# Kernel tuning notes

Hardware: AMD Instinct MI355X
Metric: run time of the kernel (lower is better)

Reference implementation:

```python
import math
import jax, jax.numpy as jnp
import numpy as np

# CoordinateDescentRouter defaults (lucidrains/CoLT5-attention)
N_ITERS, EPS, EPS_INIT, EPS_DECAY, FETCH_K_RATIO = 20, 0.03, 4.0, 0.7, 9.0 / 8.0

B, N, D, G, H, DH, NQ, NKV = 2, 4096, 1024, 2, 16, 64, 1024, 1024
DIM_INNER = H * DH  # 1024


def coor_descent(s, k):
    # s: (b, g, n). Differentiable top-k relaxation via coordinate descent.
    logk = math.log(k)
    eps_sched = [max(EPS_INIT * EPS_DECAY ** i, EPS) for i in range(N_ITERS + 1)]
    b = -s
    a = jnp.zeros_like(s[..., :1])
    for ce in eps_sched[:-1]:
        sb = (s + b) / ce
        a = ce * (logk - jax.scipy.special.logsumexp(sb, axis=-1, keepdims=True))
        b = -jax.nn.relu(s + a)
    return jnp.exp((s + a + b) / eps_sched[-1])


def route(x, routing_tokens, num_tokens):
    # x: (b,n,d), routing_tokens: (g,d) -> indices (b,g,nt), scores (b,g,nt), routed (b,g,nt,d)
    bsz, n, _ = x.shape
    k_cd = min(int(num_tokens * FETCH_K_RATIO), n)
    sim = jnp.einsum('bnd,gd->bgn', x, routing_tokens)
    scores = coor_descent(sim, k_cd)
    scores, idx = jax.lax.top_k(scores, num_tokens)
    # straight-through: forward value 1.0, gradient flows through coor_descent scores
    scores = scores + jax.lax.stop_gradient(1.0 - scores)
    routed = x[jnp.arange(bsz)[:, None, None], idx]
    return idx, scores, routed


def rmsnorm(t, gamma):
    # t: (b,g,n,d); F.normalize over feature dim * sqrt(d) * gamma (g,d)
    norm = jnp.sqrt(jnp.sum(t * t, axis=-1, keepdims=True))
    return t / jnp.maximum(norm, 1e-12) * math.sqrt(t.shape[-1]) * gamma[None, :, None, :]


def grouped_attention(queries, kvs, v_scale, o_scale, gamma_q, gamma_c, wq, wkv, wo, null_kv):
    bsz, g, nq, d = queries.shape
    h, dh = null_kv.shape[2], null_kv.shape[-1]
    qn = rmsnorm(queries, gamma_q)
    cn = rmsnorm(kvs, gamma_c)
    # grouped 1x1 conv == per-group linear; within-group output channel order is (h, dh)
    q = jnp.einsum('bgnd,ged->bgne', qn, wq)
    kv = jnp.einsum('bgnd,ged->bgne', cn, wkv)
    k, v = jnp.split(kv, 2, axis=-1)

    def to_heads(t):
        return t.reshape(bsz, g, t.shape[2], h, dh).transpose(0, 1, 3, 2, 4)  # (b,g,h,n,dh)

    q, k, v = map(to_heads, (q, k, v))
    v = v * v_scale  # (b,g,1,nkv,1) broadcast, applied before null kv concat
    nk = jnp.broadcast_to(null_kv[0][None], (bsz,) + null_kv[0].shape)
    nv = jnp.broadcast_to(null_kv[1][None], (bsz,) + null_kv[1].shape)
    k = jnp.concatenate([nk, k], axis=-2)
    v = jnp.concatenate([nv, v], axis=-2)
    sim = jnp.einsum('bghnd,bghmd->bghnm', q * dh ** -0.5, k)
    attn = jax.nn.softmax(sim, axis=-1)
    o = jnp.einsum('bghnm,bghmd->bghnd', attn, v)
    o = o.transpose(0, 1, 3, 2, 4).reshape(bsz, g, nq, h * dh)
    o = jnp.einsum('bgne,gde->bgnd', o, wo)
    return o * o_scale


def setup_inputs() -> dict:
    key = jax.random.key(0)
    ks = jax.random.split(key, 8)
    inv = 1.0 / math.sqrt(D)
    return {
        'x': jax.random.normal(ks[0], (B, N, D), jnp.float32),
        'rt_q': jax.random.normal(ks[1], (G, D), jnp.float32),
        'rt_kv': jax.random.normal(ks[2], (G, D), jnp.float32),
        'gamma_q': jnp.ones((G, D), jnp.float32),
        'gamma_c': jnp.ones((G, D), jnp.float32),
        'wq': jax.random.normal(ks[3], (G, DIM_INNER, D), jnp.float32) * inv,
        'wkv': jax.random.normal(ks[4], (G, 2 * DIM_INNER, D), jnp.float32) * inv,
        'wo': jax.random.normal(ks[5], (G, D, DIM_INNER), jnp.float32) * inv,
        'null_kv': jax.random.normal(ks[6], (2, G, H, 1, DH), jnp.float32),
        'null_token': jax.random.normal(ks[7], (1, 1, D), jnp.float32),
        'num_routed_queries': NQ,
        'num_routed_key_values': NKV,
    }


def reference(x, rt_q, rt_kv, gamma_q, gamma_c, wq, wkv, wo, null_kv, null_token,
              num_routed_queries, num_routed_key_values):
    bsz, n, d = x.shape
    q_idx, q_scores, queries = route(x, rt_q, num_routed_queries)
    _, kv_scores, key_values = route(x, rt_kv, num_routed_key_values)
    v_scale = kv_scores[:, :, None, :, None]  # (b,g,1,nkv,1)
    o_scale = q_scores[..., None]             # (b,g,nq,1)
    attn_out = grouped_attention(queries, key_values, v_scale, o_scale,
                                 gamma_q, gamma_c, wq, wkv, wo, null_kv)
    # scatter routed outputs back, averaging over experts that picked each token
    flat_idx = q_idx.reshape(bsz, -1)                 # (b, g*nq)
    flat_out = attn_out.reshape(bsz, -1, d)           # (b, g*nq, d)
    bidx = jnp.arange(bsz)[:, None]
    summed = jnp.zeros_like(x).at[bidx, flat_idx].add(flat_out)
    counts = jnp.zeros((bsz, n), x.dtype).at[bidx, flat_idx].add(1.0)
    not_routed = (counts == 0.0)[..., None]
    summed = jnp.where(not_routed, 0.0, summed)
    out = summed / jnp.maximum(counts[..., None], 1e-5)
    out = jnp.where(not_routed, null_token, out)
    return out
```

## Files before the change

### kernel.cpp

```cpp
#include <hip/hip_runtime.h>

typedef __attribute__((ext_vector_type(8))) short short8;
typedef __attribute__((ext_vector_type(4))) short short4v;
typedef __attribute__((ext_vector_type(4))) float f32x4;

#define B_ 2
#define N_ 4096
#define D_ 1024
#define G_ 2
#define H_ 16
#define DH_ 64
#define NSLOT 1088
#define LOGK 7.0492548412558374f
#define ATTN_SCALE 0.18033688011112043f
#define FIXED_M 32.0f

#define BAR() __builtin_amdgcn_s_barrier()
#define WAITV4 asm volatile("s_waitcnt vmcnt(4)" ::: "memory")
#define WAITV0 asm volatile("s_waitcnt vmcnt(0)" ::: "memory")
#define GLDS(src, dst) __builtin_amdgcn_global_load_lds( \
    (const __attribute__((address_space(1))) void*)(src), \
    (__attribute__((address_space(3))) void*)(dst), 16, 0, 0)

__device__ __forceinline__ float bf2f(short s) {
  return __uint_as_float(((unsigned)(unsigned short)s) << 16);
}
__device__ __forceinline__ short f2bf(float f) {
  unsigned u = __float_as_uint(f);
  u = (u + 0x7FFFu + ((u >> 16) & 1u)) >> 16;
  return (short)u;
}
__device__ __forceinline__ short f2bf_trunc(float f) {
  return (short)(__float_as_uint(f) >> 16);
}

__global__ __launch_bounds__(256) void prep_kernel(
    const float* __restrict__ x, const float* __restrict__ rtq,
    const float* __restrict__ rtkv, float* __restrict__ sim,
    const float* __restrict__ null_kv, short* __restrict__ kb_,
    short* __restrict__ vb_)
{
  int bid = blockIdx.x;
  if (bid < 2048) {
    int wid = threadIdx.x >> 6, lane = threadIdx.x & 63;
    int row = bid * 4 + wid;
    int b = row >> 12, n = row & (N_ - 1);
    const float* xr = x + (size_t)row * D_;
    float a0 = 0.f, a1 = 0.f, a2 = 0.f, a3 = 0.f;
#pragma unroll
    for (int c = 0; c < 4; ++c) {
      int d = c * 256 + lane * 4;
      f32x4 xv = *(const f32x4*)(xr + d);
      f32x4 r0 = *(const f32x4*)(rtq + d);
      f32x4 r1 = *(const f32x4*)(rtq + D_ + d);
      f32x4 r2 = *(const f32x4*)(rtkv + d);
      f32x4 r3 = *(const f32x4*)(rtkv + D_ + d);
#pragma unroll
      for (int e = 0; e < 4; ++e) {
        a0 += xv[e] * r0[e];
        a1 += xv[e] * r1[e];
        a2 += xv[e] * r2[e];
        a3 += xv[e] * r3[e];
      }
    }
#pragma unroll
    for (int o = 32; o; o >>= 1) {
      a0 += __shfl_xor(a0, o); a1 += __shfl_xor(a1, o);
      a2 += __shfl_xor(a2, o); a3 += __shfl_xor(a3, o);
    }
    if (lane == 0) {
      sim[((size_t)(b)*G_ + 0) * N_ + n] = a0;
      sim[((size_t)(b)*G_ + 1) * N_ + n] = a1;
      sim[((size_t)(B_ + b)*G_ + 0) * N_ + n] = a2;
      sim[((size_t)(B_ + b)*G_ + 1) * N_ + n] = a3;
    }
  } else {
    int bgh = (bid - 2048) * 4 + (threadIdx.x >> 6);
    int g = (bgh >> 4) & 1, h = bgh & 15;
    int t = threadIdx.x & 63;
    float kvk = null_kv[((size_t)(0 * G_ + g) * H_ + h) * DH_ + t];
    float kvv = null_kv[((size_t)(1 * G_ + g) * H_ + h) * DH_ + t];
    kb_[((size_t)bgh * NSLOT + 1024) * DH_ + t] = f2bf(kvk);
    vb_[((size_t)bgh * DH_ + t) * NSLOT + 1024] = f2bf(kvv);
  }
}

__global__ __launch_bounds__(1024) void topk_wconv(
    const float* __restrict__ sim, int* __restrict__ idxout, int* __restrict__ inv,
    const float* __restrict__ wq, const float* __restrict__ wkv,
    const float* __restrict__ wo, short* __restrict__ dq,
    short* __restrict__ dkv, short* __restrict__ dwo)
{
  if (blockIdx.x >= 8) {
    int base = (blockIdx.x - 8) * 4096 + threadIdx.x;
#pragma unroll
    for (int c = 0; c < 4; ++c) {
      int i = base + c * 1024;
      const float* src; short* dst;
      if (i < 524288) { src = wq; dst = dq; }
      else if (i < 1572864) { src = wkv; dst = dkv; i -= 524288; }
      else { src = wo; dst = dwo; i -= 1572864; }
      f32x4 v = ((const f32x4*)src)[i];
      short4v o;
#pragma unroll
      for (int e = 0; e < 4; ++e) o[e] = f2bf(v[e]);
      ((short4v*)dst)[i] = o;
    }
    return;
  }

  __shared__ float rbm[16];
  __shared__ float rbs[16];
  __shared__ float res;
  __shared__ unsigned keys[N_];
  __shared__ int scanbuf[16];

  int r = blockIdx.x >> 2, b = (blockIdx.x >> 1) & 1, g = blockIdx.x & 1;
  const float* srow = sim + ((size_t)blockIdx.x << 12);
  int tid = threadIdx.x, lane = tid & 63, wid = tid >> 6;

  float sv[4];
#pragma unroll
  for (int j = 0; j < 4; ++j) sv[j] = srow[tid * 4 + j];

  float a = 0.f;
  double epsd = 4.0;
  for (int it = 0; it < 20; ++it) {
    float eps = (float)fmax(epsd, 0.03);
    epsd *= 0.7;
    float sb[4]; float mt = -INFINITY;
#pragma unroll
    for (int j = 0; j < 4; ++j) {
      float bb = (it == 0) ? (-sv[j]) : (-fmaxf(sv[j] + a, 0.f));
      sb[j] = (sv[j] + bb) / eps;
      mt = fmaxf(mt, sb[j]);
    }
#pragma unroll
    for (int o = 32; o; o >>= 1) mt = fmaxf(mt, __shfl_xor(mt, o));
    float st = 0.f;
#pragma unroll
    for (int j = 0; j < 4; ++j) st += expf(sb[j] - mt);
#pragma unroll
    for (int o = 32; o; o >>= 1) st += __shfl_xor(st, o);
    if (lane == 0) { rbm[wid] = mt; rbs[wid] = st; }
    __syncthreads();
    if (tid < 64) {
      float m2 = (tid < 16) ? rbm[tid] : -INFINITY;
      float s2 = (tid < 16) ? rbs[tid] : 0.f;
#pragma unroll
      for (int o = 8; o; o >>= 1) {
        float mo = __shfl_xor(m2, o), so = __shfl_xor(s2, o);
        float mn = fmaxf(m2, mo);
        s2 = s2 * expf(m2 - mn) + so * expf(mo - mn);
        m2 = mn;
      }
      if (tid == 0) res = logf(s2) + m2;
    }
    __syncthreads();
    float lse = res;
    a = eps * (LOGK - lse);
  }
  __syncthreads();

  unsigned kb[4]; int c1 = 0;
#pragma unroll
  for (int j = 0; j < 4; ++j) {
    float sc = expf(fminf(sv[j] + a, 0.f) / 0.03f);
    kb[j] = __float_as_uint(sc);
    keys[tid * 4 + j] = kb[j];
    c1 += (kb[j] == 0x3F800000u);
  }
#pragma unroll
  for (int o = 32; o; o >>= 1) c1 += __shfl_xor(c1, o);
  if (lane == 0) scanbuf[wid] = c1;
  __syncthreads();
  int c1tot = 0;
  for (int i = 0; i < 16; ++i) c1tot += scanbuf[i];
  __syncthreads();

  int flag[4];
  if (c1tot >= 1024) {
#pragma unroll
    for (int j = 0; j < 4; ++j) flag[j] = (kb[j] == 0x3F800000u);
  } else {
#pragma unroll
    for (int j = 0; j < 4; ++j) {
      unsigned kn = kb[j]; int n = tid * 4 + j; int rank = 0;
      for (int m = 0; m < N_; ++m) {
        unsigned km = keys[m];
        rank += (km > kn) || (km == kn && m < n);
      }
      flag[j] = (rank < 1024);
    }
  }

  int cnt = flag[0] + flag[1] + flag[2] + flag[3];
  int inc = cnt;
#pragma unroll
  for (int o = 1; o < 64; o <<= 1) {
    int tt = __shfl_up(inc, o);
    if (lane >= o) inc += tt;
  }
  if (lane == 63) scanbuf[wid] = inc;
  __syncthreads();
  int off = 0;
  for (int w = 0; w < wid; ++w) off += scanbuf[w];
  int pos = off + inc - cnt;
  int* op = idxout + ((size_t)blockIdx.x << 10);
  int* ip = inv + ((size_t)(b * G_ + g) << 12);
#pragma unroll
  for (int j = 0; j < 4; ++j) {
    if (flag[j]) {
      if (pos < 1024) {
        int n = tid * 4 + j;
        op[pos] = n;
        if (r == 0) ip[n] = pos;
      }
      pos++;
    }
  }
}

__global__ __launch_bounds__(256) void gather_rms(
    const float* __restrict__ x, const int* __restrict__ idx,
    const float* __restrict__ gamma_q, const float* __restrict__ gamma_c,
    short* __restrict__ qn, short* __restrict__ cn)
{
  __shared__ float rb[4];
  __shared__ float tot;
  int id = blockIdx.x;
  int r = id >> 12, rem = id & 4095;
  int g = (rem >> 10) & 1;
  int b = rem >> 11;
  int tok = idx[id];
  int t = threadIdx.x;
  const float* xr = x + ((size_t)b * N_ + tok) * D_;
  f32x4 v = *(const f32x4*)(xr + t * 4);
  float ss = v[0]*v[0] + v[1]*v[1] + v[2]*v[2] + v[3]*v[3];
#pragma unroll
  for (int o = 32; o; o >>= 1) ss += __shfl_xor(ss, o);
  if ((t & 63) == 0) rb[t >> 6] = ss;
  __syncthreads();
  if (t == 0) tot = rb[0] + rb[1] + rb[2] + rb[3];
  __syncthreads();
  float scale = 32.0f / fmaxf(sqrtf(tot), 1e-12f);
  const float* gm = (r ? gamma_c : gamma_q) + g * D_;
  f32x4 gv = *(const f32x4*)(gm + t * 4);
  short* dst = (r ? cn : qn) + ((size_t)rem << 10) + t * 4;
  short4v ov;
#pragma unroll
  for (int e = 0; e < 4; ++e) ov[e] = f2bf(v[e] * scale * gv[e]);
  *(short4v*)dst = ov;
}

__global__ __launch_bounds__(256, 3) void gemm_qkv(
    const short* __restrict__ qn, const short* __restrict__ cn,
    const short* __restrict__ wqb, const short* __restrict__ wkvb,
    short* __restrict__ qout, short* __restrict__ kout, short* __restrict__ vout)
{
  __shared__ short As[8192];
  __shared__ short Bs[8192];
  int t = threadIdx.x, lane = t & 63, wid = t >> 6;
  int grp = lane >> 4, l15 = lane & 15;
  int wm = wid >> 1, wn = wid & 1;
  int lin = blockIdx.x + 8 * (blockIdx.y + 24 * blockIdx.z);
  int s = (lin & 7) * 96 + (lin >> 3);
  int bx = s & 7, ny = (s >> 3) % 24, bg = s / 192;
  bool isq = ny < 8;
  const short* A  = isq ? qn : cn;
  const short* Bw = isq ? wqb : wkvb;
  int NB = isq ? 1024 : 2048;
  int nbase = (isq ? ny : ny - 8) * 128;
  float oscale = isq ? ATTN_SCALE : 1.0f;
  int mbase = bx * 128;
  int g = bg & 1;
  const short* Ab = A + ((size_t)bg << 20);
  const short* Bp = Bw + ((size_t)g * NB + nbase) * 1024;

  f32x4 zero = {0.f, 0.f, 0.f, 0.f};
  f32x4 acc[4][4];
#pragma unroll
  for (int i = 0; i < 4; ++i)
#pragma unroll
    for (int j = 0; j < 4; ++j) acc[i][j] = zero;

  const short* apA[4]; const short* apB[4]; int dstoff[4];
#pragma unroll
  for (int c = 0; c < 4; ++c) {
    int u = c * 256 + t;
    int row = u >> 3, j = u & 7;
    int cu = (j ^ (row & 7)) << 3;
    apA[c] = Ab + ((size_t)(mbase + row) << 10) + cu;
    apB[c] = Bp + ((size_t)row << 10) + cu;
    dstoff[c] = c * 2048 + wid * 512;
  }

  for (int kb = 0; kb < 16; ++kb) {
    int ko = kb * 64;
    if (kb) __syncthreads();
#pragma unroll
    for (int c = 0; c < 4; ++c) {
      GLDS(apA[c] + ko, As + dstoff[c]);
      GLDS(apB[c] + ko, Bs + dstoff[c]);
    }
    WAITV0;
    __syncthreads();
    const char* Ac = (const char*)As;
    const char* Bc = (const char*)Bs;
#pragma unroll
    for (int kf = 0; kf < 2; ++kf) {
      short8 af[4], bf_[4];
#pragma unroll
      for (int mt = 0; mt < 4; ++mt) {
        int ra = wm * 64 + mt * 16 + l15;
        af[mt] = *(const short8*)(Ac + ra * 128 + (((grp << 4) + (kf << 6)) ^ ((ra & 7) << 4)));
      }
#pragma unroll
      for (int nt = 0; nt < 4; ++nt) {
        int rb = wn * 64 + nt * 16 + l15;
        bf_[nt] = *(const short8*)(Bc + rb * 128 + (((grp << 4) + (kf << 6)) ^ ((rb & 7) << 4)));
      }
      __builtin_amdgcn_s_setprio(1);
#pragma unroll
      for (int mt = 0; mt < 4; ++mt)
#pragma unroll
        for (int nt = 0; nt < 4; ++nt)
          acc[mt][nt] = __builtin_amdgcn_mfma_f32_16x16x32_bf16(af[mt], bf_[nt], acc[mt][nt], 0, 0, 0);
      __builtin_amdgcn_s_setprio(0);
    }
  }

#pragma unroll
  for (int mt = 0; mt < 4; ++mt)
#pragma unroll
    for (int nt = 0; nt < 4; ++nt) {
      int n = nbase + wn*64 + nt*16 + l15;
#pragma unroll
      for (int rr = 0; rr < 4; ++rr) {
        int m = mbase + wm*64 + mt*16 + grp*4 + rr;
        float v = acc[mt][nt][rr] * oscale;
        if (isq) {
          qout[((size_t)bg * 1024 + m) * 1024 + n] = f2bf(v);
        } else {
          if (n < 1024) {
            kout[(((size_t)bg * H_ + (n >> 6)) * NSLOT + m) * DH_ + (n & 63)] = f2bf(v);
          } else {
            int e = n - 1024;
            vout[(((size_t)bg * H_ + (e >> 6)) * DH_ + (e & 63)) * NSLOT + m] = f2bf(v);
          }
        }
      }
    }
}

__global__ __launch_bounds__(256, 3) void gemm_wo(
    const short* __restrict__ A, const short* __restrict__ Bw,
    short* __restrict__ out0, short* __restrict__ out1)
{
  __shared__ short As[8192];
  __shared__ short Bs[8192];
  int t = threadIdx.x, lane = t & 63, wid = t >> 6;
  int grp = lane >> 4, l15 = lane & 15;
  int wm = wid >> 1, wn = wid & 1;
  int lin = blockIdx.x + 8 * (blockIdx.y + 8 * blockIdx.z);
  int s = (lin & 7) * 64 + (lin >> 3);
  int mbase = (s & 7) * 128, nbase = ((s >> 3) & 7) * 128;
  int z = s >> 6, bg = z >> 1, sp = z & 1, g = bg & 1;
  short* out = sp ? out1 : out0;
  const short* Ab = A + ((size_t)bg << 20);
  const short* Bp = Bw + ((size_t)g * 1024 + nbase) * 1024;

  f32x4 zero = {0.f, 0.f, 0.f, 0.f};
  f32x4 acc[4][4];
#pragma unroll
  for (int i = 0; i < 4; ++i)
#pragma unroll
    for (int j = 0; j < 4; ++j) acc[i][j] = zero;

  const short* apA[4]; const short* apB[4]; int dstoff[4];
#pragma unroll
  for (int c = 0; c < 4; ++c) {
    int u = c * 256 + t;
    int row = u >> 3, j = u & 7;
    int cu = (j ^ (row & 7)) << 3;
    apA[c] = Ab + ((size_t)(mbase + row) << 10) + cu;
    apB[c] = Bp + ((size_t)row << 10) + cu;
    dstoff[c] = c * 2048 + wid * 512;
  }

  int kb0 = sp * 8;
  for (int kk = 0; kk < 8; ++kk) {
    int ko = (kb0 + kk) * 64;
    if (kk) __syncthreads();
#pragma unroll
    for (int c = 0; c < 4; ++c) {
      GLDS(apA[c] + ko, As + dstoff[c]);
      GLDS(apB[c] + ko, Bs + dstoff[c]);
    }
    WAITV0;
    __syncthreads();
    const char* Ac = (const char*)As;
    const char* Bc = (const char*)Bs;
#pragma unroll
    for (int kf = 0; kf < 2; ++kf) {
      short8 af[4], bf_[4];
#pragma unroll
      for (int mt = 0; mt < 4; ++mt) {
        int ra = wm * 64 + mt * 16 + l15;
        af[mt] = *(const short8*)(Ac + ra * 128 + (((grp << 4) + (kf << 6)) ^ ((ra & 7) << 4)));
      }
#pragma unroll
      for (int nt = 0; nt < 4; ++nt) {
        int rb = wn * 64 + nt * 16 + l15;
        bf_[nt] = *(const short8*)(Bc + rb * 128 + (((grp << 4) + (kf << 6)) ^ ((rb & 7) << 4)));
      }
      __builtin_amdgcn_s_setprio(1);
#pragma unroll
      for (int mt = 0; mt < 4; ++mt)
#pragma unroll
        for (int nt = 0; nt < 4; ++nt)
          acc[mt][nt] = __builtin_amdgcn_mfma_f32_16x16x32_bf16(af[mt], bf_[nt], acc[mt][nt], 0, 0, 0);
      __builtin_amdgcn_s_setprio(0);
    }
  }

#pragma unroll
  for (int mt = 0; mt < 4; ++mt)
#pragma unroll
    for (int nt = 0; nt < 4; ++nt) {
      int n = nbase + wn*64 + nt*16 + l15;
#pragma unroll
      for (int rr = 0; rr < 4; ++rr) {
        int m = mbase + wm*64 + mt*16 + grp*4 + rr;
        out[((size_t)bg * 1024 + m) * 1024 + n] = f2bf(acc[mt][nt][rr]);
      }
    }
}

__global__ __launch_bounds__(256, 3) void attn_kernel(
    const short* __restrict__ q, const short* __restrict__ k,
    const short* __restrict__ vT, short* __restrict__ o0,
    short* __restrict__ o1, float* __restrict__ ml)
{
  __shared__ short Ks[2][4096];
  __shared__ short Vs[2][4096];
  __shared__ short Ps[4][32 * 72];
  int bgh = blockIdx.x, qb = blockIdx.y, sp = blockIdx.z;
  int bg = bgh >> 4, h = bgh & 15;
  int wid = threadIdx.x >> 6, lane = threadIdx.x & 63;
  int l15 = lane & 15, grp = lane >> 4;
  int qbase = qb * 128 + wid * 32;
  short* Pw = &Ps[wid][0];

  short8 bq[2][2];
#pragma unroll
  for (int qh = 0; qh < 2; ++qh) {
    const short* qp = q + ((size_t)bg * 1024 + qbase + qh * 16 + l15) * 1024 + h * 64 + (grp << 3);
    bq[qh][0] = *(const short8*)qp;
    bq[qh][1] = *(const short8*)(qp + 32);
  }
  short8 ones8;
  short ov = (l15 == 0) ? (short)0x3F80 : (short)0;
#pragma unroll
  for (int e = 0; e < 8; ++e) ones8[e] = ov;

  int u0 = wid * 128 + lane, u1 = u0 + 64;
  int r0 = u0 >> 3, j0 = u0 & 7, r1 = u1 >> 3, j1 = u1 & 7;
  const short* kbase = k + (size_t)bgh * NSLOT * DH_;
  const short* vbase = vT + (size_t)bgh * DH_ * NSLOT;
  const short* kss0 = kbase + r0 * 64 + ((j0 ^ (r0 & 7)) << 3);
  const short* kss1 = kbase + r1 * 64 + ((j1 ^ (r1 & 7)) << 3);
  const short* vss0 = vbase + (size_t)r0 * NSLOT + ((j0 ^ (r0 & 7)) << 3);
  const short* vss1 = vbase + (size_t)r1 * NSLOT + ((j1 ^ (r1 & 7)) << 3);

  f32x4 zero = {0.f, 0.f, 0.f, 0.f};
  f32x4 minit = {-FIXED_M, -FIXED_M, -FIXED_M, -FIXED_M};
  f32x4 oacc[2][4], lacc[2];
#pragma unroll
  for (int qh = 0; qh < 2; ++qh) {
    lacc[qh] = zero;
#pragma unroll
    for (int dt = 0; dt < 4; ++dt) oacc[qh][dt] = zero;
  }

  auto STAGE = [&](int tile, int p) {
    size_t ko = (size_t)tile * 4096;
    size_t vo = (size_t)tile * 64;
    short* kd = &Ks[p][0] + wid * 1024;
    short* vd = &Vs[p][0] + wid * 1024;
    GLDS(kss0 + ko, kd);
    GLDS(kss1 + ko, kd + 512);
    GLDS(vss0 + vo, vd);
    GLDS(vss1 + vo, vd + 512);
  };

  auto PROCESS = [&](int tile, int p) {
    const char* Kc = (const char*)&Ks[p][0];
    const char* Vc = (const char*)&Vs[p][0];
    f32x4 sacc[2][4];
#pragma unroll
    for (int qh = 0; qh < 2; ++qh)
#pragma unroll
      for (int kt = 0; kt < 4; ++kt) sacc[qh][kt] = minit;
#pragma unroll
    for (int kf = 0; kf < 2; ++kf) {
      short8 ka[4];
#pragma unroll
      for (int kt = 0; kt < 4; ++kt) {
        int ra = kt * 16 + l15;
        ka[kt] = *(const short8*)(Kc + ra * 128 + (((grp + 4 * kf) ^ (ra & 7)) << 4));
      }
      __builtin_amdgcn_s_setprio(1);
#pragma unroll
      for (int kt = 0; kt < 4; ++kt)
#pragma unroll
        for (int qh = 0; qh < 2; ++qh)
          sacc[qh][kt] = __builtin_amdgcn_mfma_f32_16x16x32_bf16(ka[kt], bq[qh][kf], sacc[qh][kt], 0, 0, 0);
      __builtin_amdgcn_s_setprio(0);
    }
    if (tile == 16) {
#pragma unroll
      for (int qh = 0; qh < 2; ++qh)
#pragma unroll
        for (int kt = 0; kt < 4; ++kt)
#pragma unroll
          for (int rr = 0; rr < 4; ++rr)
            if ((kt * 16 + (grp << 2) + rr) != 0) sacc[qh][kt][rr] = -INFINITY;
    }
#pragma unroll
    for (int qh = 0; qh < 2; ++qh)
#pragma unroll
      for (int kt = 0; kt < 4; ++kt) {
        short4v pk;
#pragma unroll
        for (int rr = 0; rr < 4; ++rr) pk[rr] = f2bf_trunc(exp2f(sacc[qh][kt][rr]));
        *(short4v*)(Pw + (qh * 16 + l15) * 72 + kt * 16 + (grp << 2)) = pk;
      }
#pragma unroll
    for (int ks = 0; ks < 2; ++ks) {
      short8 pa[2];
#pragma unroll
      for (int qh = 0; qh < 2; ++qh)
        pa[qh] = *(const short8*)((const char*)Pw + (qh * 16 + l15) * 144 + grp * 16 + ks * 64);
      __builtin_amdgcn_s_setprio(1);
#pragma unroll
      for (int dt = 0; dt < 4; ++dt) {
        int ra = dt * 16 + l15;
        short8 vbf = *(const short8*)(Vc + ra * 128 + (((grp + 4 * ks) ^ (ra & 7)) << 4));
#pragma unroll
        for (int qh = 0; qh < 2; ++qh)
          oacc[qh][dt] = __builtin_amdgcn_mfma_f32_16x16x32_bf16(pa[qh], vbf, oacc[qh][dt], 0, 0, 0);
      }
#pragma unroll
      for (int qh = 0; qh < 2; ++qh)
        lacc[qh] = __builtin_amdgcn_mfma_f32_16x16x32_bf16(pa[qh], ones8, lacc[qh], 0, 0, 0);
      __builtin_amdgcn_s_setprio(0);
    }
  };

  int t0 = sp ? 8 : 0, t1 = sp ? 17 : 8;
  STAGE(t0, 0);
  STAGE(t0 + 1, 1);
  WAITV4;
  BAR();
  for (int tile = t0; tile < t1; ++tile) {
    int p = (tile - t0) & 1;
    PROCESS(tile, p);
    if (tile + 1 < t1) {
      BAR();
      if (tile + 2 < t1) { STAGE(tile + 2, p); WAITV4; }
      else               { WAITV0; }
      BAR();
    }
  }

  if (l15 == 0) {
#pragma unroll
    for (int qh = 0; qh < 2; ++qh)
#pragma unroll
      for (int rr = 0; rr < 4; ++rr)
        ml[(size_t)(sp * 64 + bgh) * 1024 + qbase + qh * 16 + (grp << 2) + rr] = lacc[qh][rr];
  }
#pragma unroll
  for (int qh = 0; qh < 2; ++qh)
#pragma unroll
    for (int dt = 0; dt < 4; ++dt)
#pragma unroll
      for (int rr = 0; rr < 4; ++rr) {
        int qq = qh * 16 + (grp << 2) + rr;
        int dh = dt * 16 + l15;
        if (sp == 0)
          o0[((size_t)bg * 1024 + qbase + qq) * 1024 + h * 64 + dh] = f2bf(oacc[qh][dt][rr]);
        else
          o1[((size_t)bgh * 1024 + qbase + qq) * 64 + dh] = f2bf(oacc[qh][dt][rr]);
      }
}

__global__ __launch_bounds__(256) void attn_merge(
    short* __restrict__ obuf, const short* __restrict__ op1,
    const float* __restrict__ ml)
{
  int id = blockIdx.x;
  int bgh = id >> 4, qc = id & 15;
  int bg = bgh >> 4, h = bgh & 15;
  int t = threadIdx.x;
  int qq = t >> 2, c = t & 3;
  int qrow = qc * 64 + qq;
  float l0 = ml[(size_t)bgh * 1024 + qrow];
  float l1 = ml[(size_t)(64 + bgh) * 1024 + qrow];
  float w = 1.0f / (l0 + l1);
  size_t loc0 = ((size_t)bg * 1024 + qrow) * 1024 + h * 64 + c * 16;
  size_t loc1 = ((size_t)bgh * 1024 + qrow) * 64 + c * 16;
  short8 a0 = *(const short8*)(obuf + loc0);
  short8 a1 = *(const short8*)(obuf + loc0 + 8);
  short8 b0 = *(const short8*)(op1 + loc1);
  short8 b1 = *(const short8*)(op1 + loc1 + 8);
  short8 r0, r1;
#pragma unroll
  for (int e = 0; e < 8; ++e) {
    r0[e] = f2bf((bf2f(a0[e]) + bf2f(b0[e])) * w);
    r1[e] = f2bf((bf2f(a1[e]) + bf2f(b1[e])) * w);
  }
  *(short8*)(obuf + loc0) = r0;
  *(short8*)(obuf + loc0 + 8) = r1;
}

__global__ __launch_bounds__(256) void finalize_kernel(
    const short* __restrict__ wo0, const short* __restrict__ wo1,
    const int* __restrict__ inv, const float* __restrict__ null_token,
    float* __restrict__ outp)
{
  int id = blockIdx.x;
  int b = id >> 12, n = id & (N_ - 1);
  int s0 = inv[((size_t)(b * G_ + 0) << 12) + n];
  int s1 = inv[((size_t)(b * G_ + 1) << 12) + n];
  int t = threadIdx.x;
  float* dst = outp + (size_t)id * D_ + t * 4;
  if (s0 < 0 && s1 < 0) {
    *(f32x4*)dst = *(const f32x4*)(null_token + t * 4);
  } else {
    f32x4 sum = {0.f, 0.f, 0.f, 0.f};
    float cnt = 0.f;
    if (s0 >= 0) {
      size_t loc = (((size_t)(b * G_ + 0) * 1024 + s0) << 10) + t * 4;
      short4v v = *(const short4v*)(wo0 + loc);
      short4v v2 = *(const short4v*)(wo1 + loc);
#pragma unroll
      for (int e = 0; e < 4; ++e) sum[e] += bf2f(v[e]) + bf2f(v2[e]);
      cnt += 1.f;
    }
    if (s1 >= 0) {
      size_t loc = (((size_t)(b * G_ + 1) * 1024 + s1) << 10) + t * 4;
      short4v v = *(const short4v*)(wo0 + loc);
      short4v v2 = *(const short4v*)(wo1 + loc);
#pragma unroll
      for (int e = 0; e < 4; ++e) sum[e] += bf2f(v[e]) + bf2f(v2[e]);
      cnt += 1.f;
    }
    f32x4 rv;
#pragma unroll
    for (int e = 0; e < 4; ++e) rv[e] = sum[e] / cnt;
    *(f32x4*)dst = rv;
  }
}

extern "C" void kernel_launch(void* const* d_in, const int* in_sizes, int n_in,
                              void* d_out, int out_size, void* d_ws, size_t ws_size,
                              hipStream_t stream) {
  (void)in_sizes; (void)n_in; (void)out_size; (void)ws_size;
  const float* x        = (const float*)d_in[0];
  const float* rt_q     = (const float*)d_in[1];
  const float* rt_kv    = (const float*)d_in[2];
  const float* gamma_q  = (const float*)d_in[3];
  const float* gamma_c  = (const float*)d_in[4];
  const float* wq       = (const float*)d_in[5];
  const float* wkv      = (const float*)d_in[6];
  const float* wo       = (const float*)d_in[7];
  const float* null_kv  = (const float*)d_in[8];
  const float* null_tok = (const float*)d_in[9];
  float* outp = (float*)d_out;

  char* ws = (char*)d_ws;
  size_t off = 0;
  auto alloc = [&](size_t bytes) { char* p = ws + off; off += (bytes + 255) & ~(size_t)255; return p; };
  float* sim   = (float*)alloc((size_t)2 * B_ * G_ * N_ * 4);
  int*   idx   = (int*)  alloc((size_t)2 * B_ * G_ * 1024 * 4);
  int*   inv   = (int*)  alloc((size_t)B_ * G_ * N_ * 4);
  float* ml    = (float*)alloc((size_t)2 * 64 * 1024 * 4);
  short* qn    = (short*)alloc((size_t)B_ * G_ * 1024 * 1024 * 2);
  short* cn    = (short*)alloc((size_t)B_ * G_ * 1024 * 1024 * 2);
  short* qproj = (short*)alloc((size_t)B_ * G_ * 1024 * 1024 * 2);
  size_t kvbytes = (size_t)B_ * G_ * H_ * NSLOT * DH_ * 2;
  short* kbuf  = (short*)alloc(kvbytes);
  short* vbuf  = (short*)alloc(kvbytes);
  short* obuf  = (short*)alloc((size_t)B_ * G_ * 1024 * 1024 * 2);
  short* wobuf = (short*)alloc((size_t)B_ * G_ * 1024 * 1024 * 2);
  short* wo_bf = (short*)alloc((size_t)G_ * 1024 * 1024 * 2);
  short* wq_bf  = wobuf;
  short* wkv_bf = obuf;
  short* op1    = cn;
  short* wobuf2 = qproj;

  hipMemsetAsync(inv, 0xFF, (size_t)B_ * G_ * N_ * 4, stream);

  prep_kernel<<<2064, 256, 0, stream>>>(x, rt_q, rt_kv, sim, null_kv, kbuf, vbuf);
  topk_wconv<<<520, 1024, 0, stream>>>(sim, idx, inv, wq, wkv, wo,
                                       wq_bf, wkv_bf, wo_bf);
  gather_rms<<<2 * B_ * G_ * 1024, 256, 0, stream>>>(x, idx, gamma_q, gamma_c, qn, cn);
  gemm_qkv<<<dim3(8, 24, B_ * G_), 256, 0, stream>>>(qn, cn, wq_bf, wkv_bf, qproj, kbuf, vbuf);
  attn_kernel<<<dim3(64, 8, 2), 256, 0, stream>>>(qproj, kbuf, vbuf, obuf, op1, ml);
  attn_merge<<<1024, 256, 0, stream>>>(obuf, op1, ml);
  gemm_wo<<<dim3(8, 8, 2 * B_ * G_), 256, 0, stream>>>(obuf, wo_bf, wobuf, wobuf2);
  finalize_kernel<<<B_ * N_, 256, 0, stream>>>(wobuf, wobuf2, inv, null_tok, outp);
}
```

Baseline: 164.9 us.

## Drop split-KV attention and merge kernel; normalize output in-kernel

Each attention block now processes all 17 KV tiles itself instead of splitting them across two blocks. It normalizes its output by the row sum directly, which removes the attn_merge kernel, the partial-output buffer and the ml buffer traffic. The cost is that the grid halves to 512 blocks with twice the serial work each, which lowers parallelism on a GPU with many CUs.

```diff
diff --git a/kernel.cpp b/kernel.cpp
--- a/kernel.cpp
+++ b/kernel.cpp
@@ -439,13 +439,12 @@
 
 __global__ __launch_bounds__(256, 3) void attn_kernel(
     const short* __restrict__ q, const short* __restrict__ k,
-    const short* __restrict__ vT, short* __restrict__ o0,
-    short* __restrict__ o1, float* __restrict__ ml)
+    const short* __restrict__ vT, short* __restrict__ o0)
 {
   __shared__ short Ks[2][4096];
   __shared__ short Vs[2][4096];
   __shared__ short Ps[4][32 * 72];
-  int bgh = blockIdx.x, qb = blockIdx.y, sp = blockIdx.z;
+  int bgh = blockIdx.x, qb = blockIdx.y;
   int bg = bgh >> 4, h = bgh & 15;
   int wid = threadIdx.x >> 6, lane = threadIdx.x & 63;
   int l15 = lane & 15, grp = lane >> 4;
@@ -558,71 +557,35 @@
     }
   };
 
-  int t0 = sp ? 8 : 0, t1 = sp ? 17 : 8;
-  STAGE(t0, 0);
-  STAGE(t0 + 1, 1);
+  STAGE(0, 0);
+  STAGE(1, 1);
   WAITV4;
   BAR();
-  for (int tile = t0; tile < t1; ++tile) {
-    int p = (tile - t0) & 1;
+  for (int tile = 0; tile < 17; ++tile) {
+    int p = tile & 1;
     PROCESS(tile, p);
-    if (tile + 1 < t1) {
+    if (tile + 1 < 17) {
       BAR();
-      if (tile + 2 < t1) { STAGE(tile + 2, p); WAITV4; }
+      if (tile + 2 < 17) { STAGE(tile + 2, p); WAITV4; }
       else               { WAITV0; }
       BAR();
     }
   }
 
-  if (l15 == 0) {
-#pragma unroll
-    for (int qh = 0; qh < 2; ++qh)
-#pragma unroll
-      for (int rr = 0; rr < 4; ++rr)
-        ml[(size_t)(sp * 64 + bgh) * 1024 + qbase + qh * 16 + (grp << 2) + rr] = lacc[qh][rr];
-  }
 #pragma unroll
   for (int qh = 0; qh < 2; ++qh)
 #pragma unroll
-    for (int dt = 0; dt < 4; ++dt)
-#pragma unroll
-      for (int rr = 0; rr < 4; ++rr) {
-        int qq = qh * 16 + (grp << 2) + rr;
+    for (int rr = 0; rr < 4; ++rr) {
+      float lv = __shfl(lacc[qh][rr], grp << 4);
+      float inv_l = 1.0f / lv;
+      int qq = qh * 16 + (grp << 2) + rr;
+#pragma unroll
+      for (int dt = 0; dt < 4; ++dt) {
         int dh = dt * 16 + l15;
-        if (sp == 0)
-          o0[((size_t)bg * 1024 + qbase + qq) * 1024 + h * 64 + dh] = f2bf(oacc[qh][dt][rr]);
-        else
-          o1[((size_t)bgh * 1024 + qbase + qq) * 64 + dh] = f2bf(oacc[qh][dt][rr]);
-      }
-}
-
-__global__ __launch_bounds__(256) void attn_merge(
-    short* __restrict__ obuf, const short* __restrict__ op1,
-    const float* __restrict__ ml)
-{
-  int id = blockIdx.x;
-  int bgh = id >> 4, qc = id & 15;
-  int bg = bgh >> 4, h = bgh & 15;
-  int t = threadIdx.x;
-  int qq = t >> 2, c = t & 3;
-  int qrow = qc * 64 + qq;
-  float l0 = ml[(size_t)bgh * 1024 + qrow];
-  float l1 = ml[(size_t)(64 + bgh) * 1024 + qrow];
-  float w = 1.0f / (l0 + l1);
-  size_t loc0 = ((size_t)bg * 1024 + qrow) * 1024 + h * 64 + c * 16;
-  size_t loc1 = ((size_t)bgh * 1024 + qrow) * 64 + c * 16;
-  short8 a0 = *(const short8*)(obuf + loc0);
-  short8 a1 = *(const short8*)(obuf + loc0 + 8);
-  short8 b0 = *(const short8*)(op1 + loc1);
-  short8 b1 = *(const short8*)(op1 + loc1 + 8);
-  short8 r0, r1;
-#pragma unroll
-  for (int e = 0; e < 8; ++e) {
-    r0[e] = f2bf((bf2f(a0[e]) + bf2f(b0[e])) * w);
-    r1[e] = f2bf((bf2f(a1[e]) + bf2f(b1[e])) * w);
-  }
-  *(short8*)(obuf + loc0) = r0;
-  *(short8*)(obuf + loc0 + 8) = r1;
+        o0[((size_t)bg * 1024 + qbase + qq) * 1024 + h * 64 + dh] =
+            f2bf(oacc[qh][dt][rr] * inv_l);
+      }
+    }
 }
 
 __global__ __launch_bounds__(256) void finalize_kernel(
@@ -686,7 +649,6 @@
   float* sim   = (float*)alloc((size_t)2 * B_ * G_ * N_ * 4);
   int*   idx   = (int*)  alloc((size_t)2 * B_ * G_ * 1024 * 4);
   int*   inv   = (int*)  alloc((size_t)B_ * G_ * N_ * 4);
-  float* ml    = (float*)alloc((size_t)2 * 64 * 1024 * 4);
   short* qn    = (short*)alloc((size_t)B_ * G_ * 1024 * 1024 * 2);
   short* cn    = (short*)alloc((size_t)B_ * G_ * 1024 * 1024 * 2);
   short* qproj = (short*)alloc((size_t)B_ * G_ * 1024 * 1024 * 2);
@@ -698,7 +660,6 @@
   short* wo_bf = (short*)alloc((size_t)G_ * 1024 * 1024 * 2);
   short* wq_bf  = wobuf;
   short* wkv_bf = obuf;
-  short* op1    = cn;
   short* wobuf2 = qproj;
 
   hipMemsetAsync(inv, 0xFF, (size_t)B_ * G_ * N_ * 4, stream);
@@ -708,8 +669,7 @@
                                        wq_bf, wkv_bf, wo_bf);
   gather_rms<<<2 * B_ * G_ * 1024, 256, 0, stream>>>(x, idx, gamma_q, gamma_c, qn, cn);
   gemm_qkv<<<dim3(8, 24, B_ * G_), 256, 0, stream>>>(qn, cn, wq_bf, wkv_bf, qproj, kbuf, vbuf);
-  attn_kernel<<<dim3(64, 8, 2), 256, 0, stream>>>(qproj, kbuf, vbuf, obuf, op1, ml);
-  attn_merge<<<1024, 256, 0, stream>>>(obuf, op1, ml);
+  attn_kernel<<<dim3(64, 8), 256, 0, stream>>>(qproj, kbuf, vbuf, obuf);
   gemm_wo<<<dim3(8, 8, 2 * B_ * G_), 256, 0, stream>>>(obuf, wo_bf, wobuf, wobuf2);
   finalize_kernel<<<B_ * N_, 256, 0, stream>>>(wobuf, wobuf2, inv, null_tok, outp);
 }
```

Result: faster. 158.2 us (-4.1%).
